# Optimization experiments

Hardware: AMD Instinct MI355X
Metric: run time of the kernel (lower is better)

Reference implementation:

```python
import jax, jax.numpy as jnp
import numpy as np

N, E = 50000, 800000
D_IN, HID, H = 128, 64, 4
NEG_SLOPE = 0.2

def setup_inputs() -> dict:
    key = jax.random.key(0)
    ks = jax.random.split(key, 12)
    r = lambda i, shape, s=1.0: jax.random.normal(ks[i], shape, jnp.float32) * s
    return dict(
        x=r(0, (N, D_IN)),
        edge_index=jax.random.randint(ks[1], (2, E), 0, N, jnp.int32),
        W_in=r(2, (D_IN, HID), 0.05), b_in=jnp.zeros((HID,), jnp.float32),
        W1=r(3, (D_IN, H * HID), 0.05), a1_src=r(4, (H, HID), 0.05), a1_dst=r(5, (H, HID), 0.05), b1=jnp.zeros((HID,), jnp.float32),
        W2=r(6, (HID, H * HID), 0.05), a2_src=r(7, (H, HID), 0.05), a2_dst=r(8, (H, HID), 0.05), b2=jnp.zeros((HID,), jnp.float32),
        g1=jnp.ones((HID,), jnp.float32), be1=jnp.zeros((HID,), jnp.float32),
        g2=jnp.ones((HID,), jnp.float32), be2=jnp.zeros((HID,), jnp.float32),
        Wo=r(9, (HID, HID), 0.05), bo=jnp.zeros((HID,), jnp.float32),
    )

def layer_norm(x, g, b, eps=1e-5):
    mu = x.mean(-1, keepdims=True)
    var = ((x - mu) ** 2).mean(-1, keepdims=True)
    return (x - mu) * jax.lax.rsqrt(var + eps) * g + b

def gat_conv(x, W, a_src, a_dst, b, src, dst):
    # PyG GATConv, concat=False (mean over heads), self-loops already in src/dst
    n = x.shape[0]
    h = (x @ W).reshape(n, H, HID)                      # [N,H,C]
    e_src = jnp.einsum('nhc,hc->nh', h, a_src)          # [N,H]
    e_dst = jnp.einsum('nhc,hc->nh', h, a_dst)
    e = jax.nn.leaky_relu(e_src[src] + e_dst[dst], NEG_SLOPE)   # [E+N,H]
    # segment softmax over destination nodes
    m = jax.ops.segment_max(e, dst, num_segments=n)
    e = jnp.exp(e - m[dst])
    s = jax.ops.segment_sum(e, dst, num_segments=n)
    alpha = e / (s[dst] + 1e-16)                        # [E+N,H]
    msg = h[src] * alpha[:, :, None]                    # [E+N,H,C]
    out = jax.ops.segment_sum(msg, dst, num_segments=n) # [N,H,C]
    return out.mean(axis=1) + b                         # concat=False -> mean

def reference(x, W_in, b_in, W1, a1_src, a1_dst, b1, W2, a2_src, a2_dst, b2,
              g1, be1, g2, be2, Wo, bo, edge_index):
    loop = jnp.arange(N, dtype=edge_index.dtype)
    src = jnp.concatenate([edge_index[0], loop])
    dst = jnp.concatenate([edge_index[1], loop])
    residual = x @ W_in + b_in
    h = jax.nn.elu(gat_conv(x, W1, a1_src, a1_dst, b1, src, dst))
    h = layer_norm(h + residual, g1, be1)
    h2 = jax.nn.elu(gat_conv(h, W2, a2_src, a2_dst, b2, src, dst))
    h = layer_norm(h2 + h, g2, be2)
    return h @ Wo + bo
```

## Files before the change

### kernel.cpp

```cpp
#include <hip/hip_runtime.h>


using short8 = __attribute__((ext_vector_type(8))) short;
using floatx4 = __attribute__((ext_vector_type(4))) float;
using floatx2 = __attribute__((ext_vector_type(2))) float;

#define OVCAP 65536

__device__ __forceinline__ float wave_sum(float v) {
#pragma unroll
  for (int m = 32; m >= 1; m >>= 1) v += __shfl_xor(v, m, 64);
  return v;
}
__device__ __forceinline__ float wave_max(float v) {
#pragma unroll
  for (int m = 32; m >= 1; m >>= 1) v = fmaxf(v, __shfl_xor(v, m, 64));
  return v;
}
__device__ __forceinline__ unsigned pack_bf16(float lo, float hi) {
  unsigned r;
  asm volatile("v_cvt_pk_bf16_f32 %0, %1, %2" : "=v"(r) : "v"(lo), "v"(hi));
  return r;
}
__device__ __forceinline__ float bf_lo(unsigned u) { return __uint_as_float(u << 16); }
__device__ __forceinline__ float bf_hi(unsigned u) { return __uint_as_float(u & 0xffff0000u); }
__device__ __forceinline__ float lrelu(float e) { return e > 0.f ? e : 0.2f * e; }
__device__ __forceinline__ unsigned pack_fp8x4(float h0, float h1, float h2,
                                               float h3) {
  int u = __builtin_amdgcn_cvt_pk_fp8_f32(h0, h1, 0, false);
  u = __builtin_amdgcn_cvt_pk_fp8_f32(h2, h3, u, true);
  return (unsigned)u;
}

__device__ __forceinline__ void scatter_edge(const int* __restrict__ src,
                                             const int* __restrict__ dst,
                                             int* __restrict__ cnt,
                                             int* __restrict__ srcs,
                                             uint2* __restrict__ ov,
                                             int* __restrict__ ovcnt, int e) {
  int d = dst[e], s = src[e];
  int pos = atomicAdd(&cnt[d], 1);
  if (pos < 63) {
    srcs[(long)d * 64 + pos] = s;
  } else {
    int o = atomicAdd(ovcnt, 1);
    if (o < OVCAP) ov[o] = make_uint2((unsigned)s, (unsigned)d);
  }
}

__device__ __forceinline__ float waDot(const float* W, const float* a, int k,
                                       int h) {
  float s = 0.f;
#pragma unroll 8
  for (int c = 0; c < 64; ++c) s += W[k * 256 + h * 64 + c] * a[h * 64 + c];
  return s;
}
__device__ __forceinline__ void pack_body(
    int t, int l, const float* __restrict__ W1, const float* __restrict__ Win,
    const float* __restrict__ a1s, const float* __restrict__ a1d,
    const float* __restrict__ W2, const float* __restrict__ a2s,
    const float* __restrict__ a2d, const float* __restrict__ Wo,
    ushort* __restrict__ Bpk1, ushort* __restrict__ Bpk2,
    ushort* __restrict__ Bpk3) {
  const int l15 = l & 15, lhi = l >> 4;
  float w[8];
  ushort* dstp;
  if (t < 84) {
    const int kt = t / 21, nt = t - kt * 21;
    const int kb = kt * 32 + lhi * 8, col = nt * 16 + l15;
#pragma unroll
    for (int e = 0; e < 8; ++e) {
      int k = kb + e;
      float v = 0.f;
      if (col < 256) v = W1[k * 256 + col];
      else if (col < 320) v = Win[k * 64 + (col - 256)];
      else if (col < 324) v = waDot(W1, a1s, k, col - 320);
      else if (col < 328) v = waDot(W1, a1d, k, col - 324);
      w[e] = v;
    }
    dstp = Bpk1 + ((long)t * 64 + l) * 8;
  } else if (t < 120) {
    const int t2 = t - 84;
    if (t2 >= 34) return;
    const int kt = t2 / 17, nt = t2 - kt * 17;
    const int kb = kt * 32 + lhi * 8, col = nt * 16 + l15;
#pragma unroll
    for (int e = 0; e < 8; ++e) {
      int k = kb + e;
      float v = 0.f;
      if (col < 256) v = W2[k * 256 + col];
      else if (col < 260) v = waDot(W2, a2s, k, col - 256);
      else if (col < 264) v = waDot(W2, a2d, k, col - 260);
      w[e] = v;
    }
    dstp = Bpk2 + ((long)t2 * 64 + l) * 8;
  } else {
    const int t3 = t - 120;
    if (t3 >= 8) return;
    const int kt = t3 / 4, nt = t3 - kt * 4;
    const int kb = kt * 32 + lhi * 8, col = nt * 16 + l15;
#pragma unroll
    for (int e = 0; e < 8; ++e) w[e] = Wo[(kb + e) * 64 + col];
    dstp = Bpk3 + ((long)t3 * 64 + l) * 8;
  }
  uint4 o;
  o.x = pack_bf16(w[0], w[1]);
  o.y = pack_bf16(w[2], w[3]);
  o.z = pack_bf16(w[4], w[5]);
  o.w = pack_bf16(w[6], w[7]);
  *(uint4*)dstp = o;
}

template <int KA, int KT, int NT, int MODE>
__device__ __forceinline__ void gemm_body(
    const float* __restrict__ Af32, const ushort* __restrict__ Abf,
    const ushort* __restrict__ Bpk, const float* __restrict__ bias,
    unsigned* __restrict__ Hb, float* __restrict__ eSs,
    float* __restrict__ eDs, float* __restrict__ RES,
    float* __restrict__ outp, int nrows, int bid) {
  const int lane = threadIdx.x & 63;
  const int wid = threadIdx.x >> 6;
  const int row0 = (bid * 4 + wid) * 16;
  if (row0 >= nrows) return;
  const int l15 = lane & 15, lhi = lane >> 4;
  const int rowA = min(row0 + l15, nrows - 1);
  floatx4 acc[NT];
  const floatx4 zero = {0.f, 0.f, 0.f, 0.f};
#pragma unroll
  for (int nt = 0; nt < NT; ++nt) acc[nt] = zero;
#pragma unroll
  for (int kt = 0; kt < KT; ++kt) {
    short8 af;
    if (MODE == 1) {
      const float* ap = Af32 + (long)rowA * KA + lhi * 8 + kt * 32;
      float4 u = *(const float4*)ap;
      float4 v = *(const float4*)(ap + 4);
      union { unsigned u[4]; short8 s; } cv;
      cv.u[0] = pack_bf16(u.x, u.y);
      cv.u[1] = pack_bf16(u.z, u.w);
      cv.u[2] = pack_bf16(v.x, v.y);
      cv.u[3] = pack_bf16(v.z, v.w);
      af = cv.s;
    } else {
      af = *(const short8*)(Abf + (long)rowA * KA + lhi * 8 + kt * 32);
    }
    const ushort* bp = Bpk + ((long)(kt * NT) * 64 + lane) * 8;
#pragma unroll
    for (int nt = 0; nt < NT; ++nt) {
      short8 bf = *(const short8*)(bp + (long)nt * 64 * 8);
      acc[nt] = __builtin_amdgcn_mfma_f32_16x16x32_bf16(af, bf, acc[nt], 0, 0, 0);
    }
  }
#pragma unroll
  for (int reg = 0; reg < 4; ++reg) {
    const int node = row0 + lhi * 4 + reg;
    if (node >= nrows) continue;
    if (MODE == 1 || MODE == 2) {
#pragma unroll
      for (int nt = 0; nt < 4; ++nt) {
        Hb[(long)node * 64 + nt * 16 + l15] =
            pack_fp8x4(acc[nt][reg], acc[nt + 4][reg], acc[nt + 8][reg],
                       acc[nt + 12][reg]);
      }
      if (MODE == 1) {
#pragma unroll
        for (int nt = 16; nt < 20; ++nt) {
          int col = (nt - 16) * 16 + l15;
          RES[(long)node * 64 + col] = acc[nt][reg] + bias[col];
        }
      }
      constexpr int ET = (MODE == 1) ? 20 : 16;
      float ev = acc[ET][reg];
      if (l15 < 4) eSs[node * 4 + l15] = ev;
      else if (l15 < 8) eDs[node * 4 + (l15 - 4)] = ev;
    } else {
#pragma unroll
      for (int nt = 0; nt < NT; ++nt) {
        int col = nt * 16 + l15;
        outp[(long)node * 64 + col] = acc[nt][reg] + bias[col];
      }
    }
  }
}

__global__ __launch_bounds__(256) void pack_scatter_kernel(
    const float* __restrict__ W1, const float* __restrict__ Win,
    const float* __restrict__ a1s, const float* __restrict__ a1d,
    const float* __restrict__ W2, const float* __restrict__ a2s,
    const float* __restrict__ a2d, const float* __restrict__ Wo,
    ushort* __restrict__ Bpk1, ushort* __restrict__ Bpk2,
    ushort* __restrict__ Bpk3, const int* __restrict__ src,
    const int* __restrict__ dst, int* __restrict__ cnt,
    int* __restrict__ srcs, uint2* __restrict__ ov, int* __restrict__ ovcnt,
    int Eh) {
  const int b = blockIdx.x;
  if (b < 32) {
    pack_body(b * 4 + (threadIdx.x >> 6), threadIdx.x & 63, W1, Win, a1s, a1d,
              W2, a2s, a2d, Wo, Bpk1, Bpk2, Bpk3);
    return;
  }
  int e = (b - 32) * 256 + threadIdx.x;
  if (e < Eh) scatter_edge(src, dst, cnt, srcs, ov, ovcnt, e);
}

__global__ __launch_bounds__(256) void gemm1_scatter_kernel(
    const float* __restrict__ Af32, const ushort* __restrict__ Bpk1,
    const float* __restrict__ bias, unsigned* __restrict__ Hb,
    float* __restrict__ eSs, float* __restrict__ eDs, float* __restrict__ RES,
    int nrows, int gemmBlocks, const int* __restrict__ src,
    const int* __restrict__ dst, int* __restrict__ cnt,
    int* __restrict__ srcs, uint2* __restrict__ ov, int* __restrict__ ovcnt,
    int Eh, int E) {
  const int b = blockIdx.x;
  if (b < gemmBlocks) {
    gemm_body<128, 4, 21, 1>(Af32, nullptr, Bpk1, bias, Hb, eSs, eDs, RES,
                             nullptr, nrows, b);
    return;
  }
  int e = Eh + (b - gemmBlocks) * 256 + threadIdx.x;
  if (e < E) scatter_edge(src, dst, cnt, srcs, ov, ovcnt, e);
}

template <int KA, int KT, int NT, int MODE>
__global__ __launch_bounds__(256) void mfma_gemm_kernel(
    const float* __restrict__ Af32, const ushort* __restrict__ Abf,
    const ushort* __restrict__ Bpk, const float* __restrict__ bias,
    unsigned* __restrict__ Hb, float* __restrict__ eSs,
    float* __restrict__ eDs, float* __restrict__ RES,
    float* __restrict__ outp, int nrows) {
  gemm_body<KA, KT, NT, MODE>(Af32, Abf, Bpk, bias, Hb, eSs, eDs, RES, outp,
                              nrows, blockIdx.x);
}

__global__ __launch_bounds__(256) void agg_kernel(
    const int* __restrict__ cnt, const int* __restrict__ srcs,
    const unsigned* __restrict__ Hb, const float4* __restrict__ eS,
    const float4* __restrict__ eD, const float* __restrict__ bias,
    const float* __restrict__ resid, const float* __restrict__ gamma,
    const float* __restrict__ beta, float* __restrict__ out,
    ushort* __restrict__ outbf, const uint2* __restrict__ ov,
    const int* __restrict__ ovcnt, int n) {
  const int lane = threadIdx.x & 63;
  const int node = blockIdx.x * 4 + (threadIdx.x >> 6);
  if (node >= n) return;
  const int deg = cnt[node];
  const int start = node * 64;
  const float4 ed = eD[node];

  float a0 = 0.f, a1 = 0.f, a2 = 0.f, a3 = 0.f;

  if (deg <= 63) {
    const int slot = max(0, min(lane - 1, deg - 1));
    const int sv = srcs[start + slot];
    const int sj = (lane == 0 || lane > deg) ? node : sv;
    const bool act = lane <= deg;
    const float4 es = eS[sj];
    float e0 = lrelu(es.x + ed.x), e1 = lrelu(es.y + ed.y);
    float e2 = lrelu(es.z + ed.z), e3 = lrelu(es.w + ed.w);
    float em = fmaxf(fmaxf(e0, e1), fmaxf(e2, e3));
    float M = wave_max(act ? em : -1e30f);
    float p0 = act ? __expf(e0 - M) : 0.f;
    float p1 = act ? __expf(e1 - M) : 0.f;
    float p2 = act ? __expf(e2 - M) : 0.f;
    float p3 = act ? __expf(e3 - M) : 0.f;
    float s0 = wave_sum(p0), s1 = wave_sum(p1);
    float s2 = wave_sum(p2), s3 = wave_sum(p3);
    p0 *= 1.f / (s0 + 1e-16f);
    p1 *= 1.f / (s1 + 1e-16f);
    p2 *= 1.f / (s2 + 1e-16f);
    p3 *= 1.f / (s3 + 1e-16f);
    const unsigned apk01 = pack_bf16(p0, p1);
    const unsigned apk23 = pack_bf16(p2, p3);

    const int cntUp = (deg + 4) & ~3;
#define LOADJ(dstv, jj)                                   \
  {                                                       \
    int s_ = __builtin_amdgcn_readlane(sj, (jj));         \
    const unsigned* b_ = Hb + ((size_t)(unsigned)s_ << 6);\
    dstv = b_[lane];                                      \
  }
#define CONSJ(hv, jj)                                                     \
  {                                                                       \
    unsigned q01 = __builtin_amdgcn_readlane(apk01, (jj));                \
    unsigned q23 = __builtin_amdgcn_readlane(apk23, (jj));                \
    floatx2 l01 = __builtin_amdgcn_cvt_pk_f32_fp8((int)hv, false);        \
    floatx2 l23 = __builtin_amdgcn_cvt_pk_f32_fp8((int)hv, true);         \
    a0 = fmaf(bf_lo(q01), l01.x, a0);                                     \
    a1 = fmaf(bf_hi(q01), l01.y, a1);                                     \
    a2 = fmaf(bf_lo(q23), l23.x, a2);                                     \
    a3 = fmaf(bf_hi(q23), l23.y, a3);                                     \
  }
    unsigned hA, hB, hC, hD;
    LOADJ(hA, 0) LOADJ(hB, 1) LOADJ(hC, 2) LOADJ(hD, 3)
    int j = 0;
    for (; j + 8 <= cntUp; j += 4) {
      unsigned nA, nB, nC, nD;
      LOADJ(nA, j + 4) LOADJ(nB, j + 5) LOADJ(nC, j + 6) LOADJ(nD, j + 7)
      CONSJ(hA, j) CONSJ(hB, j + 1) CONSJ(hC, j + 2) CONSJ(hD, j + 3)
      hA = nA; hB = nB; hC = nC; hD = nD;
    }
    CONSJ(hA, j) CONSJ(hB, j + 1) CONSJ(hC, j + 2) CONSJ(hD, j + 3)
#undef LOADJ
#undef CONSJ
  } else {
    int ovn = min(*ovcnt, OVCAP);
    const int sv = (lane < 63) ? srcs[start + lane] : node;
    float4 es = eS[sv];
    float e0 = lrelu(es.x + ed.x), e1 = lrelu(es.y + ed.y);
    float e2 = lrelu(es.z + ed.z), e3 = lrelu(es.w + ed.w);
    float M0 = e0, M1 = e1, M2 = e2, M3 = e3;
    for (int i = lane; i < ovn; i += 64) {
      uint2 o = ov[i];
      if ((int)o.y == node) {
        float4 eo = eS[o.x];
        M0 = fmaxf(M0, lrelu(eo.x + ed.x));
        M1 = fmaxf(M1, lrelu(eo.y + ed.y));
        M2 = fmaxf(M2, lrelu(eo.z + ed.z));
        M3 = fmaxf(M3, lrelu(eo.w + ed.w));
      }
    }
    float m0 = wave_max(M0), m1 = wave_max(M1);
    float m2 = wave_max(M2), m3 = wave_max(M3);
    float S0 = __expf(e0 - m0), S1 = __expf(e1 - m1);
    float S2 = __expf(e2 - m2), S3 = __expf(e3 - m3);
    for (int i = lane; i < ovn; i += 64) {
      uint2 o = ov[i];
      if ((int)o.y == node) {
        float4 eo = eS[o.x];
        S0 += __expf(lrelu(eo.x + ed.x) - m0);
        S1 += __expf(lrelu(eo.y + ed.y) - m1);
        S2 += __expf(lrelu(eo.z + ed.z) - m2);
        S3 += __expf(lrelu(eo.w + ed.w) - m3);
      }
    }
    float i0 = 1.f / (wave_sum(S0) + 1e-16f), i1 = 1.f / (wave_sum(S1) + 1e-16f);
    float i2 = 1.f / (wave_sum(S2) + 1e-16f), i3 = 1.f / (wave_sum(S3) + 1e-16f);
#define ACCE(sidx)                                                        \
  {                                                                       \
    int s_ = (sidx);                                                      \
    unsigned h = Hb[(long)s_ * 64 + lane];                                \
    float4 e_ = eS[s_];                                                   \
    floatx2 l01 = __builtin_amdgcn_cvt_pk_f32_fp8((int)h, false);         \
    floatx2 l23 = __builtin_amdgcn_cvt_pk_f32_fp8((int)h, true);          \
    float al;                                                             \
    al = __expf(lrelu(e_.x + ed.x) - m0) * i0;                            \
    a0 = fmaf(al, l01.x, a0);                                             \
    al = __expf(lrelu(e_.y + ed.y) - m1) * i1;                            \
    a1 = fmaf(al, l01.y, a1);                                             \
    al = __expf(lrelu(e_.z + ed.z) - m2) * i2;                            \
    a2 = fmaf(al, l23.x, a2);                                             \
    al = __expf(lrelu(e_.w + ed.w) - m3) * i3;                            \
    a3 = fmaf(al, l23.y, a3);                                             \
  }
    for (int i = 0; i < 63; ++i) ACCE(srcs[start + i]);
    ACCE(node);
    for (int k = 0; k < ovn; ++k) {
      uint2 o = ov[k];
      if ((int)o.y == node) ACCE((int)o.x);
    }
#undef ACCE
  }

  float o = (a0 + a1 + a2 + a3) * 0.25f + bias[lane];
  o = o > 0.f ? o : (__expf(o) - 1.f);
  float v = o + resid[(long)node * 64 + lane];
  float mean = wave_sum(v) * (1.f / 64.f);
  float d = v - mean;
  float var = wave_sum(d * d) * (1.f / 64.f);
  float r = rsqrtf(var + 1e-5f);
  float res = d * r * gamma[lane] + beta[lane];
  if (out) out[(long)node * 64 + lane] = res;
  outbf[(long)node * 64 + lane] = (ushort)pack_bf16(res, res);
}

extern "C" void kernel_launch(void* const* d_in, const int* in_sizes, int n_in,
                              void* d_out, int out_size, void* d_ws,
                              size_t ws_size, hipStream_t stream) {
  const float* x    = (const float*)d_in[0];
  const int*   ei   = (const int*)d_in[1];
  const float* W_in = (const float*)d_in[2];
  const float* b_in = (const float*)d_in[3];
  const float* W1   = (const float*)d_in[4];
  const float* a1s  = (const float*)d_in[5];
  const float* a1d  = (const float*)d_in[6];
  const float* b1   = (const float*)d_in[7];
  const float* W2   = (const float*)d_in[8];
  const float* a2s  = (const float*)d_in[9];
  const float* a2d  = (const float*)d_in[10];
  const float* b2   = (const float*)d_in[11];
  const float* g1   = (const float*)d_in[12];
  const float* be1  = (const float*)d_in[13];
  const float* g2   = (const float*)d_in[14];
  const float* be2  = (const float*)d_in[15];
  const float* Wo   = (const float*)d_in[16];
  const float* bo   = (const float*)d_in[17];
  float* out = (float*)d_out;

  const int N = in_sizes[0] / 128;
  const int E = in_sizes[1] / 2;
  const int* src = ei;
  const int* dst = ei + E;

  char* p = (char*)d_ws;
  unsigned* Hb = (unsigned*)p;    p += (long)N * 64 * 4;
  float* RES   = (float*)p;       p += (long)N * 64 * 4;
  float* HL1   = (float*)p;       p += (long)N * 64 * 4;
  ushort* HLbf = (ushort*)p;      p += (long)N * 64 * 2;
  float* eSs   = (float*)p;       p += (long)N * 4 * 4;
  float* eDs   = (float*)p;       p += (long)N * 4 * 4;
  ushort* Bpk1 = (ushort*)p;      p += 84L * 64 * 8 * 2;
  ushort* Bpk2 = (ushort*)p;      p += 34L * 64 * 8 * 2;
  ushort* Bpk3 = (ushort*)p;      p += 8L * 64 * 8 * 2;
  int* cnt     = (int*)p;         p += (long)N * 4;
  int* ovcnt   = (int*)p;         p += 16;
  int* srcs    = (int*)p;         p += (long)N * 64 * 4;
  uint2* ov    = (uint2*)p;       p += (long)OVCAP * 8;

  const dim3 blk(256);
  const int nodeGrid = (N + 3) / 4;
  const int gemmBlocks = (N + 63) / 64;
  const int Eh = E / 2;

  hipMemsetAsync(cnt, 0, (long)N * 4 + 16, stream);

  pack_scatter_kernel<<<32 + (Eh + 255) / 256, blk, 0, stream>>>(
      W1, W_in, a1s, a1d, W2, a2s, a2d, Wo, Bpk1, Bpk2, Bpk3, src, dst, cnt,
      srcs, ov, ovcnt, Eh);
  gemm1_scatter_kernel<<<gemmBlocks + (E - Eh + 255) / 256, blk, 0, stream>>>(
      x, Bpk1, b_in, Hb, eSs, eDs, RES, N, gemmBlocks, src, dst, cnt, srcs,
      ov, ovcnt, Eh, E);

  agg_kernel<<<nodeGrid, blk, 0, stream>>>(
      cnt, srcs, Hb, (const float4*)eSs, (const float4*)eDs, b1, RES, g1, be1,
      HL1, HLbf, ov, ovcnt, N);

  mfma_gemm_kernel<64, 2, 17, 2><<<gemmBlocks, blk, 0, stream>>>(
      nullptr, HLbf, Bpk2, b_in, Hb, eSs, eDs, nullptr, nullptr, N);

  agg_kernel<<<nodeGrid, blk, 0, stream>>>(
      cnt, srcs, Hb, (const float4*)eSs, (const float4*)eDs, b2, HL1, g2, be2,
      nullptr, HLbf, ov, ovcnt, N);

  mfma_gemm_kernel<64, 2, 4, 3><<<gemmBlocks, blk, 0, stream>>>(
      nullptr, HLbf, Bpk3, bo, nullptr, nullptr, nullptr, nullptr, out, N);
}
```

Measured before the change: 194.9 us.

## Store edge sources as u16 and residuals in bf16, drop fp32 hidden buffer

The per-node source list is stored as 16-bit indices instead of 32-bit, and the input-projection residual is written and read as bf16 instead of fp32. The fp32 copy of the first layer's output is no longer written; the second aggregation takes its residual from the bf16 buffer and overwrites that buffer in place. The 0.25 head-mean factor is folded into the softmax normalisers. The aim is to cut memory traffic in the scatter, GEMM epilogue and aggregation kernels. The cost is lower residual precision, and the 16-bit indices only hold while the node count stays below 65536.

```diff
diff --git a/kernel.cpp b/kernel.cpp
--- a/kernel.cpp
+++ b/kernel.cpp
@@ -35,13 +35,13 @@
 __device__ __forceinline__ void scatter_edge(const int* __restrict__ src,
                                              const int* __restrict__ dst,
                                              int* __restrict__ cnt,
-                                             int* __restrict__ srcs,
+                                             ushort* __restrict__ srcs,
                                              uint2* __restrict__ ov,
                                              int* __restrict__ ovcnt, int e) {
   int d = dst[e], s = src[e];
   int pos = atomicAdd(&cnt[d], 1);
   if (pos < 63) {
-    srcs[(long)d * 64 + pos] = s;
+    srcs[(long)d * 64 + pos] = (ushort)s;
   } else {
     int o = atomicAdd(ovcnt, 1);
     if (o < OVCAP) ov[o] = make_uint2((unsigned)s, (unsigned)d);
@@ -116,7 +116,7 @@
     const float* __restrict__ Af32, const ushort* __restrict__ Abf,
     const ushort* __restrict__ Bpk, const float* __restrict__ bias,
     unsigned* __restrict__ Hb, float* __restrict__ eSs,
-    float* __restrict__ eDs, float* __restrict__ RES,
+    float* __restrict__ eDs, ushort* __restrict__ RESbf,
     float* __restrict__ outp, int nrows, int bid) {
   const int lane = threadIdx.x & 63;
   const int wid = threadIdx.x >> 6;
@@ -166,7 +166,8 @@
 #pragma unroll
         for (int nt = 16; nt < 20; ++nt) {
           int col = (nt - 16) * 16 + l15;
-          RES[(long)node * 64 + col] = acc[nt][reg] + bias[col];
+          float v = acc[nt][reg] + bias[col];
+          RESbf[(long)node * 64 + col] = (ushort)pack_bf16(v, v);
         }
       }
       constexpr int ET = (MODE == 1) ? 20 : 16;
@@ -191,8 +192,8 @@
     ushort* __restrict__ Bpk1, ushort* __restrict__ Bpk2,
     ushort* __restrict__ Bpk3, const int* __restrict__ src,
     const int* __restrict__ dst, int* __restrict__ cnt,
-    int* __restrict__ srcs, uint2* __restrict__ ov, int* __restrict__ ovcnt,
-    int Eh) {
+    ushort* __restrict__ srcs, uint2* __restrict__ ov,
+    int* __restrict__ ovcnt, int Eh) {
   const int b = blockIdx.x;
   if (b < 32) {
     pack_body(b * 4 + (threadIdx.x >> 6), threadIdx.x & 63, W1, Win, a1s, a1d,
@@ -206,14 +207,14 @@
 __global__ __launch_bounds__(256) void gemm1_scatter_kernel(
     const float* __restrict__ Af32, const ushort* __restrict__ Bpk1,
     const float* __restrict__ bias, unsigned* __restrict__ Hb,
-    float* __restrict__ eSs, float* __restrict__ eDs, float* __restrict__ RES,
-    int nrows, int gemmBlocks, const int* __restrict__ src,
-    const int* __restrict__ dst, int* __restrict__ cnt,
-    int* __restrict__ srcs, uint2* __restrict__ ov, int* __restrict__ ovcnt,
-    int Eh, int E) {
+    float* __restrict__ eSs, float* __restrict__ eDs,
+    ushort* __restrict__ RESbf, int nrows, int gemmBlocks,
+    const int* __restrict__ src, const int* __restrict__ dst,
+    int* __restrict__ cnt, ushort* __restrict__ srcs, uint2* __restrict__ ov,
+    int* __restrict__ ovcnt, int Eh, int E) {
   const int b = blockIdx.x;
   if (b < gemmBlocks) {
-    gemm_body<128, 4, 21, 1>(Af32, nullptr, Bpk1, bias, Hb, eSs, eDs, RES,
+    gemm_body<128, 4, 21, 1>(Af32, nullptr, Bpk1, bias, Hb, eSs, eDs, RESbf,
                              nullptr, nrows, b);
     return;
   }
@@ -226,20 +227,19 @@
     const float* __restrict__ Af32, const ushort* __restrict__ Abf,
     const ushort* __restrict__ Bpk, const float* __restrict__ bias,
     unsigned* __restrict__ Hb, float* __restrict__ eSs,
-    float* __restrict__ eDs, float* __restrict__ RES,
+    float* __restrict__ eDs, ushort* __restrict__ RESbf,
     float* __restrict__ outp, int nrows) {
-  gemm_body<KA, KT, NT, MODE>(Af32, Abf, Bpk, bias, Hb, eSs, eDs, RES, outp,
+  gemm_body<KA, KT, NT, MODE>(Af32, Abf, Bpk, bias, Hb, eSs, eDs, RESbf, outp,
                               nrows, blockIdx.x);
 }
 
 __global__ __launch_bounds__(256) void agg_kernel(
-    const int* __restrict__ cnt, const int* __restrict__ srcs,
+    const int* __restrict__ cnt, const ushort* __restrict__ srcs,
     const unsigned* __restrict__ Hb, const float4* __restrict__ eS,
     const float4* __restrict__ eD, const float* __restrict__ bias,
-    const float* __restrict__ resid, const float* __restrict__ gamma,
-    const float* __restrict__ beta, float* __restrict__ out,
-    ushort* __restrict__ outbf, const uint2* __restrict__ ov,
-    const int* __restrict__ ovcnt, int n) {
+    const ushort* __restrict__ residbf, const float* __restrict__ gamma,
+    const float* __restrict__ beta, ushort* __restrict__ outbf,
+    const uint2* __restrict__ ov, const int* __restrict__ ovcnt, int n) {
   const int lane = threadIdx.x & 63;
   const int node = blockIdx.x * 4 + (threadIdx.x >> 6);
   if (node >= n) return;
@@ -265,10 +265,10 @@
     float p3 = act ? __expf(e3 - M) : 0.f;
     float s0 = wave_sum(p0), s1 = wave_sum(p1);
     float s2 = wave_sum(p2), s3 = wave_sum(p3);
-    p0 *= 1.f / (s0 + 1e-16f);
-    p1 *= 1.f / (s1 + 1e-16f);
-    p2 *= 1.f / (s2 + 1e-16f);
-    p3 *= 1.f / (s3 + 1e-16f);
+    p0 *= 0.25f / (s0 + 1e-16f);
+    p1 *= 0.25f / (s1 + 1e-16f);
+    p2 *= 0.25f / (s2 + 1e-16f);
+    p3 *= 0.25f / (s3 + 1e-16f);
     const unsigned apk01 = pack_bf16(p0, p1);
     const unsigned apk23 = pack_bf16(p2, p3);
 
@@ -304,7 +304,7 @@
 #undef CONSJ
   } else {
     int ovn = min(*ovcnt, OVCAP);
-    const int sv = (lane < 63) ? srcs[start + lane] : node;
+    const int sv = (lane < 63) ? (int)srcs[start + lane] : node;
     float4 es = eS[sv];
     float e0 = lrelu(es.x + ed.x), e1 = lrelu(es.y + ed.y);
     float e2 = lrelu(es.z + ed.z), e3 = lrelu(es.w + ed.w);
@@ -333,8 +333,10 @@
         S3 += __expf(lrelu(eo.w + ed.w) - m3);
       }
     }
-    float i0 = 1.f / (wave_sum(S0) + 1e-16f), i1 = 1.f / (wave_sum(S1) + 1e-16f);
-    float i2 = 1.f / (wave_sum(S2) + 1e-16f), i3 = 1.f / (wave_sum(S3) + 1e-16f);
+    float i0 = 0.25f / (wave_sum(S0) + 1e-16f);
+    float i1 = 0.25f / (wave_sum(S1) + 1e-16f);
+    float i2 = 0.25f / (wave_sum(S2) + 1e-16f);
+    float i3 = 0.25f / (wave_sum(S3) + 1e-16f);
 #define ACCE(sidx)                                                        \
   {                                                                       \
     int s_ = (sidx);                                                      \
@@ -352,7 +354,7 @@
     al = __expf(lrelu(e_.w + ed.w) - m3) * i3;                            \
     a3 = fmaf(al, l23.y, a3);                                             \
   }
-    for (int i = 0; i < 63; ++i) ACCE(srcs[start + i]);
+    for (int i = 0; i < 63; ++i) ACCE((int)srcs[start + i]);
     ACCE(node);
     for (int k = 0; k < ovn; ++k) {
       uint2 o = ov[k];
@@ -361,15 +363,14 @@
 #undef ACCE
   }
 
-  float o = (a0 + a1 + a2 + a3) * 0.25f + bias[lane];
+  float o = a0 + a1 + a2 + a3 + bias[lane];
   o = o > 0.f ? o : (__expf(o) - 1.f);
-  float v = o + resid[(long)node * 64 + lane];
+  float v = o + bf_lo((unsigned)residbf[(long)node * 64 + lane]);
   float mean = wave_sum(v) * (1.f / 64.f);
   float d = v - mean;
   float var = wave_sum(d * d) * (1.f / 64.f);
   float r = rsqrtf(var + 1e-5f);
   float res = d * r * gamma[lane] + beta[lane];
-  if (out) out[(long)node * 64 + lane] = res;
   outbf[(long)node * 64 + lane] = (ushort)pack_bf16(res, res);
 }
 
@@ -402,19 +403,18 @@
   const int* dst = ei + E;
 
   char* p = (char*)d_ws;
-  unsigned* Hb = (unsigned*)p;    p += (long)N * 64 * 4;
-  float* RES   = (float*)p;       p += (long)N * 64 * 4;
-  float* HL1   = (float*)p;       p += (long)N * 64 * 4;
-  ushort* HLbf = (ushort*)p;      p += (long)N * 64 * 2;
-  float* eSs   = (float*)p;       p += (long)N * 4 * 4;
-  float* eDs   = (float*)p;       p += (long)N * 4 * 4;
-  ushort* Bpk1 = (ushort*)p;      p += 84L * 64 * 8 * 2;
-  ushort* Bpk2 = (ushort*)p;      p += 34L * 64 * 8 * 2;
-  ushort* Bpk3 = (ushort*)p;      p += 8L * 64 * 8 * 2;
-  int* cnt     = (int*)p;         p += (long)N * 4;
-  int* ovcnt   = (int*)p;         p += 16;
-  int* srcs    = (int*)p;         p += (long)N * 64 * 4;
-  uint2* ov    = (uint2*)p;       p += (long)OVCAP * 8;
+  unsigned* Hb  = (unsigned*)p;   p += (long)N * 64 * 4;
+  ushort* HLbf  = (ushort*)p;     p += (long)N * 64 * 2;
+  ushort* RESbf = (ushort*)p;     p += (long)N * 64 * 2;
+  float* eSs    = (float*)p;      p += (long)N * 4 * 4;
+  float* eDs    = (float*)p;      p += (long)N * 4 * 4;
+  ushort* Bpk1  = (ushort*)p;     p += 84L * 64 * 8 * 2;
+  ushort* Bpk2  = (ushort*)p;     p += 34L * 64 * 8 * 2;
+  ushort* Bpk3  = (ushort*)p;     p += 8L * 64 * 8 * 2;
+  int* cnt      = (int*)p;        p += (long)N * 4;
+  int* ovcnt    = (int*)p;        p += 16;
+  ushort* srcs  = (ushort*)p;     p += (long)N * 64 * 2;
+  uint2* ov     = (uint2*)p;      p += (long)OVCAP * 8;
 
   const dim3 blk(256);
   const int nodeGrid = (N + 3) / 4;
@@ -427,19 +427,19 @@
       W1, W_in, a1s, a1d, W2, a2s, a2d, Wo, Bpk1, Bpk2, Bpk3, src, dst, cnt,
       srcs, ov, ovcnt, Eh);
   gemm1_scatter_kernel<<<gemmBlocks + (E - Eh + 255) / 256, blk, 0, stream>>>(
-      x, Bpk1, b_in, Hb, eSs, eDs, RES, N, gemmBlocks, src, dst, cnt, srcs,
+      x, Bpk1, b_in, Hb, eSs, eDs, RESbf, N, gemmBlocks, src, dst, cnt, srcs,
       ov, ovcnt, Eh, E);
 
   agg_kernel<<<nodeGrid, blk, 0, stream>>>(
-      cnt, srcs, Hb, (const float4*)eSs, (const float4*)eDs, b1, RES, g1, be1,
-      HL1, HLbf, ov, ovcnt, N);
+      cnt, srcs, Hb, (const float4*)eSs, (const float4*)eDs, b1, RESbf, g1,
+      be1, HLbf, ov, ovcnt, N);
 
   mfma_gemm_kernel<64, 2, 17, 2><<<gemmBlocks, blk, 0, stream>>>(
       nullptr, HLbf, Bpk2, b_in, Hb, eSs, eDs, nullptr, nullptr, N);
 
   agg_kernel<<<nodeGrid, blk, 0, stream>>>(
-      cnt, srcs, Hb, (const float4*)eSs, (const float4*)eDs, b2, HL1, g2, be2,
-      nullptr, HLbf, ov, ovcnt, N);
+      cnt, srcs, Hb, (const float4*)eSs, (const float4*)eDs, b2, HLbf, g2,
+      be2, HLbf, ov, ovcnt, N);
 
   mfma_gemm_kernel<64, 2, 4, 3><<<gemmBlocks, blk, 0, stream>>>(
       nullptr, HLbf, Bpk3, bo, nullptr, nullptr, nullptr, nullptr, out, N);
```

Result: no change. 195.4 us (+0.3%).
